# Kernel tuning notes

Measured on AMD Instinct MI355X. Metric: run time of the kernel, lower is better.

## Reference

```python
import jax, jax.numpy as jnp
import numpy as np

SPEED_OF_SOUND = 343.0
SAMPLING_FREQUENCY = 96000.0
CROP_LENGTH = 256


def setup_inputs() -> dict:
    key = jax.random.key(0)
    k1, k2, k3, k4 = jax.random.split(key, 4)
    B1, B2, R, T = 4, 1024, 64, 16384
    recordings = jax.random.normal(k1, (B1, R, T), dtype=jnp.float32)
    sample_locations = jax.random.uniform(k2, (B1, B2, 3), dtype=jnp.float32)  # points in unit cube
    emitter_location = jnp.array([0.0, 0.0, 0.5], dtype=jnp.float32)
    receiver_locations = jax.random.uniform(k3, (R, 3), dtype=jnp.float32) * 0.2
    canonical_echo = jax.random.normal(k4, (CROP_LENGTH,), dtype=jnp.float32)
    return {
        "recordings": recordings,
        "sample_locations": sample_locations,
        "emitter_location": emitter_location,
        "receiver_locations": receiver_locations,
        "canonical_echo": canonical_echo,
    }


def _time_of_flight_crop(recordings, sample_locations, emitter_location, receiver_locations):
    # recordings: (B1, R, T); sample_locations: (B1, B2, 3)
    B1, R, T = recordings.shape
    # emitter -> sample distance: (B1, B2)
    d_es = jnp.linalg.norm(sample_locations - emitter_location, axis=-1)
    # sample -> receiver distance: (B1, B2, R)
    d_sr = jnp.linalg.norm(
        sample_locations[:, :, None, :] - receiver_locations[None, None, :, :], axis=-1
    )
    # fractional start sample index of the echo window: (B1, B2, R)
    start = (d_es[:, :, None] + d_sr) / SPEED_OF_SOUND * SAMPLING_FREQUENCY
    # fractional sample indices for the crop window: (B1, B2, R, L)
    idx = start[..., None] + jnp.arange(CROP_LENGTH, dtype=recordings.dtype)
    i0f = jnp.floor(idx)
    frac = idx - i0f
    i0 = jnp.clip(i0f.astype(jnp.int32), 0, T - 1)
    i1 = jnp.clip(i0 + 1, 0, T - 1)
    # gather per (B1, R) row: vmap over B2 so we never broadcast recordings to (B1,B2,R,T)
    gather = jax.vmap(
        lambda i: jnp.take_along_axis(recordings, i, axis=-1), in_axes=1, out_axes=1
    )
    v0 = gather(i0)  # (B1, B2, R, L)
    v1 = gather(i1)
    return v0 * (1.0 - frac) + v1 * frac  # linear interpolation


def reference(recordings, sample_locations, emitter_location, receiver_locations, canonical_echo):
    cropped = _time_of_flight_crop(
        recordings, sample_locations, emitter_location, receiver_locations
    )  # (B1, B2, R, L)
    # dot with canonical echo template over L, clamp at 0, sum over receivers
    products = jnp.einsum("bqrl,l->bqr", cropped, canonical_echo)
    products = jnp.maximum(products, 0.0)
    magnitude = jnp.sum(products, axis=2)  # (B1, B2)
    return magnitude
```

## Files before the change

### kernel.cpp

```cpp
#include <hip/hip_runtime.h>

#define T_LEN 16384
#define R_CNT 64
#define CROP 256
#define B2_CNT 1024
#define CDW 588
#define CDW_S 664
#define NLAG 928

typedef _Float16 h2 __attribute__((ext_vector_type(2)));

__device__ __forceinline__ h2 as_h2(unsigned u) {
    union { unsigned u; h2 h; } v; v.u = u; return v.h;
}

#if __has_builtin(__builtin_amdgcn_fdot2)
__device__ __forceinline__ float DOT2(unsigned a, unsigned b, float c) {
    return __builtin_amdgcn_fdot2(as_h2(a), as_h2(b), c, false);
}
#else
__device__ __forceinline__ float DOT2(unsigned a, unsigned b, float c) {
    h2 x = as_h2(a), y = as_h2(b);
    return fmaf((float)x[0], (float)y[0], fmaf((float)x[1], (float)y[1], c));
}
#endif

__global__ __launch_bounds__(256) void corr_kernel(
    const float* __restrict__ recordings,
    const float* __restrict__ echo,
    float* __restrict__ C)
{
    const int blk  = blockIdx.x;
    const int b1   = blk >> 8;
    const int r    = (blk >> 2) & 63;
    const int base = (blk & 3) * 256;
    const int tid  = threadIdx.x;
    const int lane = tid & 63;
    const int wave = tid >> 6;
    const int i8   = lane & 7;
    const int g3   = lane >> 3;

    __shared__ __align__(16) unsigned s_copy[8 * CDW_S];
    __shared__ __align__(16) unsigned s_echo_pk[CROP / 2];

    const float* __restrict__ row = recordings + ((size_t)b1 * R_CNT + r) * T_LEN;
    #pragma unroll
    for (int c = 0; c < 8; ++c)
        for (int j = tid; j < CDW; j += 256) {
            const float a = row[c + 2 * j];
            const float b = row[c + 2 * j + 1];
            s_copy[c * CDW_S + j + 4 * (j >> 5)] =
                __builtin_bit_cast(unsigned, __builtin_amdgcn_cvt_pkrtz(a, b));
        }
    if (tid < CROP / 2)
        s_echo_pk[tid] = __builtin_bit_cast(unsigned,
            __builtin_amdgcn_cvt_pkrtz(echo[2 * tid], echo[2 * tid + 1]));
    __syncthreads();

    unsigned e[16];
    #pragma unroll
    for (int n = 0; n < 4; ++n)
        *(uint4*)&e[4 * n] = *(const uint4*)&s_echo_pk[i8 * 16 + 4 * n];

    const int s = wave * 8 + g3;
    float* __restrict__ Crow = C + ((size_t)b1 * R_CNT + r) * NLAG;

    #pragma unroll
    for (int pass = 0; pass < 4; ++pass) {
        const int J = base + pass * 64 + (s & 7) + ((s >> 3) * 16);
        if (J < 920) {
            const int c = J & 7;
            const int b = J >> 3;
            const unsigned* __restrict__ cb = &s_copy[c * CDW_S];

            unsigned d[20];
            #pragma unroll
            for (int n = 0; n < 5; ++n) {
                const int dj = 4 * b + 16 * i8 + 4 * n;
                *(uint4*)&d[4 * n] = *(const uint4*)&cb[dj + 4 * (dj >> 5)];
            }

            float a0 = 0.0f, a1 = 0.0f;
            #pragma unroll
            for (int k = 0; k < 16; ++k) {
                a0 = DOT2(e[k], d[k],     a0);
                a1 = DOT2(e[k], d[k + 4], a1);
            }
            a0 += __shfl_xor(a0, 1); a1 += __shfl_xor(a1, 1);
            a0 += __shfl_xor(a0, 2); a1 += __shfl_xor(a1, 2);
            a0 += __shfl_xor(a0, 4); a1 += __shfl_xor(a1, 4);
            if (i8 == 0) {
                Crow[J]     = a0;
                Crow[J + 8] = a1;
            }
        }
    }
}

__global__ __launch_bounds__(256) void pair_kernel(
    const float* __restrict__ sample_locations,
    const float* __restrict__ emitter,
    const float* __restrict__ receivers,
    const float* __restrict__ C,
    float* __restrict__ out)
{
    const int blk = blockIdx.x;
    const int b1  = blk >> 6;
    const int qc  = blk & 63;
    const int tid = threadIdx.x;
    const int ql  = tid & 15;
    const int rg  = tid >> 4;

    __shared__ float s_recv[R_CNT * 3];
    __shared__ float s_part[16][17];

    if (tid < R_CNT * 3) s_recv[tid] = receivers[tid];
    __syncthreads();

    const int q = qc * 16 + ql;
    const float sx = sample_locations[(b1 * B2_CNT + q) * 3 + 0];
    const float sy = sample_locations[(b1 * B2_CNT + q) * 3 + 1];
    const float sz = sample_locations[(b1 * B2_CNT + q) * 3 + 2];
    const float ex = emitter[0], ey = emitter[1], ez = emitter[2];
    const float dex = sx - ex, dey = sy - ey, dez = sz - ez;
    const float d_es = sqrtf(fmaf(dex, dex, fmaf(dey, dey, dez * dez)));

    const float SCALE = 96000.0f / 343.0f;
    float acc = 0.0f;

    #pragma unroll
    for (int rr = 0; rr < 4; ++rr) {
        const int r = rg * 4 + rr;
        const float rx = s_recv[r * 3 + 0];
        const float ry = s_recv[r * 3 + 1];
        const float rz = s_recv[r * 3 + 2];
        const float dx = sx - rx, dy = sy - ry, dz = sz - rz;
        const float d_sr = sqrtf(fmaf(dx, dx, fmaf(dy, dy, dz * dz)));

        const float start = (d_es + d_sr) * SCALE;
        const float i0f   = floorf(start);
        const float frac  = start - i0f;
        int s0 = (int)i0f;
        s0 = s0 < 0 ? 0 : (s0 > 904 ? 904 : s0);

        const float* cp = C + ((size_t)b1 * R_CNT + r) * NLAG + s0;
        const float c0 = cp[0];
        const float c1 = cp[1];
        acc += fmaxf(fmaf(frac, c1 - c0, c0), 0.0f);
    }

    s_part[rg][ql] = acc;
    __syncthreads();

    if (tid < 16) {
        float sum = 0.0f;
        #pragma unroll
        for (int g = 0; g < 16; ++g) sum += s_part[g][tid];
        out[b1 * B2_CNT + qc * 16 + tid] = sum;
    }
}

extern "C" void kernel_launch(void* const* d_in, const int* in_sizes, int n_in,
                              void* d_out, int out_size, void* d_ws, size_t ws_size,
                              hipStream_t stream) {
    const float* recordings       = (const float*)d_in[0];
    const float* sample_locations = (const float*)d_in[1];
    const float* emitter          = (const float*)d_in[2];
    const float* receivers        = (const float*)d_in[3];
    const float* echo             = (const float*)d_in[4];
    float* out                    = (float*)d_out;
    float* C                      = (float*)d_ws;

    const int B1 = in_sizes[1] / (B2_CNT * 3);

    corr_kernel<<<dim3(B1 * R_CNT * 4), dim3(256), 0, stream>>>(recordings, echo, C);
    pair_kernel<<<dim3(B1 * 64), dim3(256), 0, stream>>>(sample_locations, emitter,
                                                         receivers, C, out);
}
```

Baseline: 77.70 us.

## Stage only each block's quarter of the row and compute four lags per thread

Each block now loads into shared memory only the slice of the recording row its 256 lags need (about 260 packed words per phase instead of 588), which cuts redundant global reads and fp16 conversions across the four blocks sharing a row. The inner loop now produces four lag outputs per thread in two passes instead of two outputs in four passes, so each shared-memory data load and echo register is reused more. This needs more registers (28 data words, four accumulators), and the bounds checks move to the stores.

```diff
diff --git a/kernel.cpp b/kernel.cpp
--- a/kernel.cpp
+++ b/kernel.cpp
@@ -4,8 +4,8 @@
 #define R_CNT 64
 #define CROP 256
 #define B2_CNT 1024
-#define CDW 588
-#define CDW_S 664
+#define CDW_Q 260
+#define CDW_QS 296
 #define NLAG 928
 
 typedef _Float16 h2 __attribute__((ext_vector_type(2)));
@@ -40,16 +40,16 @@
     const int i8   = lane & 7;
     const int g3   = lane >> 3;
 
-    __shared__ __align__(16) unsigned s_copy[8 * CDW_S];
+    __shared__ __align__(16) unsigned s_copy[8 * CDW_QS];
     __shared__ __align__(16) unsigned s_echo_pk[CROP / 2];
 
-    const float* __restrict__ row = recordings + ((size_t)b1 * R_CNT + r) * T_LEN;
+    const float* __restrict__ row = recordings + ((size_t)b1 * R_CNT + r) * T_LEN + base;
     #pragma unroll
     for (int c = 0; c < 8; ++c)
-        for (int j = tid; j < CDW; j += 256) {
+        for (int j = tid; j < CDW_Q; j += 256) {
             const float a = row[c + 2 * j];
             const float b = row[c + 2 * j + 1];
-            s_copy[c * CDW_S + j + 4 * (j >> 5)] =
+            s_copy[c * CDW_QS + j + 4 * (j >> 5)] =
                 __builtin_bit_cast(unsigned, __builtin_amdgcn_cvt_pkrtz(a, b));
         }
     if (tid < CROP / 2)
@@ -66,33 +66,40 @@
     float* __restrict__ Crow = C + ((size_t)b1 * R_CNT + r) * NLAG;
 
     #pragma unroll
-    for (int pass = 0; pass < 4; ++pass) {
-        const int J = base + pass * 64 + (s & 7) + ((s >> 3) * 16);
-        if (J < 920) {
-            const int c = J & 7;
-            const int b = J >> 3;
-            const unsigned* __restrict__ cb = &s_copy[c * CDW_S];
+    for (int pass = 0; pass < 2; ++pass) {
+        const int Jl = (s & 7) + ((s >> 3) * 32) + pass * 128;
+        const int c  = Jl & 7;
+        const int b  = Jl >> 3;
+        const unsigned* __restrict__ cb = &s_copy[c * CDW_QS];
 
-            unsigned d[20];
-            #pragma unroll
-            for (int n = 0; n < 5; ++n) {
-                const int dj = 4 * b + 16 * i8 + 4 * n;
-                *(uint4*)&d[4 * n] = *(const uint4*)&cb[dj + 4 * (dj >> 5)];
-            }
+        unsigned d[28];
+        #pragma unroll
+        for (int n = 0; n < 7; ++n) {
+            const int dj = 4 * b + 16 * i8 + 4 * n;
+            *(uint4*)&d[4 * n] = *(const uint4*)&cb[dj + 4 * (dj >> 5)];
+        }
 
-            float a0 = 0.0f, a1 = 0.0f;
-            #pragma unroll
-            for (int k = 0; k < 16; ++k) {
-                a0 = DOT2(e[k], d[k],     a0);
-                a1 = DOT2(e[k], d[k + 4], a1);
-            }
-            a0 += __shfl_xor(a0, 1); a1 += __shfl_xor(a1, 1);
-            a0 += __shfl_xor(a0, 2); a1 += __shfl_xor(a1, 2);
-            a0 += __shfl_xor(a0, 4); a1 += __shfl_xor(a1, 4);
-            if (i8 == 0) {
-                Crow[J]     = a0;
-                Crow[J + 8] = a1;
-            }
+        float a0 = 0.0f, a1 = 0.0f, a2 = 0.0f, a3 = 0.0f;
+        #pragma unroll
+        for (int k = 0; k < 16; ++k) {
+            a0 = DOT2(e[k], d[k],      a0);
+            a1 = DOT2(e[k], d[k + 4],  a1);
+            a2 = DOT2(e[k], d[k + 8],  a2);
+            a3 = DOT2(e[k], d[k + 12], a3);
+        }
+        #pragma unroll
+        for (int off = 1; off <= 4; off <<= 1) {
+            a0 += __shfl_xor(a0, off);
+            a1 += __shfl_xor(a1, off);
+            a2 += __shfl_xor(a2, off);
+            a3 += __shfl_xor(a3, off);
+        }
+        if (i8 == 0) {
+            const int J = base + Jl;
+            if (J      < 920) Crow[J]      = a0;
+            if (J + 8  < 920) Crow[J + 8]  = a1;
+            if (J + 16 < 920) Crow[J + 16] = a2;
+            if (J + 24 < 920) Crow[J + 24] = a3;
         }
     }
 }
```

New measurement: 74.58 us. 1.04x faster.
